# Kernel optimization log

Hardware: AMD Instinct MI355X
Metric: run time of the kernel (lower is better)

## Reference

```python
import jax, jax.numpy as jnp
import numpy as np

NUM_QUBITS = 4
NUM_LAYERS = 3
B = 16384


def ry(t):
    # t: scalar or [B] -> [2,2] or [B,2,2] complex64
    c = jnp.cos(t / 2)
    s = jnp.sin(t / 2)
    return jnp.stack([jnp.stack([c, -s], -1), jnp.stack([s, c], -1)], -2).astype(jnp.complex64)


def rz(t):
    e = jnp.exp(-0.5j * t.astype(jnp.complex64))
    z = jnp.zeros_like(e)
    return jnp.stack([jnp.stack([e, z], -1), jnp.stack([z, jnp.conj(e)], -1)], -2)


def apply_gate(psi, G, wire):
    # psi: [B,2,2,2,2]; G: [2,2] (shared) or [B,2,2] (per-sample)
    ax = 1 + wire
    psi = jnp.moveaxis(psi, ax, -1)
    if G.ndim == 3:
        psi = jnp.einsum('b...j,bij->b...i', psi, G)
    else:
        psi = jnp.einsum('...j,ij->...i', psi, G)
    return jnp.moveaxis(psi, -1, ax)


def cnot(psi, c, t):
    ca, ta = 1 + c, 1 + t
    p0 = jnp.take(psi, 0, axis=ca)
    p1 = jnp.take(psi, 1, axis=ca)
    p1 = jnp.flip(p1, axis=ta - (1 if ta > ca else 0))
    return jnp.stack([p0, p1], axis=ca)


def quantum_layer(inputs, qw):
    # inputs: [B,4] angles; qw: [3,4,2] circuit weights -> [B,4] PauliZ expvals
    b = inputs.shape[0]
    psi = jnp.zeros((b, 2, 2, 2, 2), jnp.complex64).at[:, 0, 0, 0, 0].set(1.0)
    for w in range(NUM_QUBITS):
        psi = apply_gate(psi, ry(inputs[:, w]), w)
    for l in range(NUM_LAYERS):
        for q in range(NUM_QUBITS):
            psi = apply_gate(psi, ry(qw[l, q, 0]), q)
            psi = apply_gate(psi, rz(qw[l, q, 1]), q)
        for q in range(NUM_QUBITS - 1):
            psi = cnot(psi, q, q + 1)
        psi = cnot(psi, NUM_QUBITS - 1, 0)
    pr = jnp.real(psi * jnp.conj(psi))  # [B,2,2,2,2]
    signs = jnp.array([1.0, -1.0], jnp.float32)
    outs = []
    for w in range(NUM_QUBITS):
        shp = [1, 1, 1, 1, 1]
        shp[1 + w] = 2
        outs.append(jnp.sum(pr * signs.reshape(shp), axis=(1, 2, 3, 4)))
    return jnp.stack(outs, axis=1).astype(jnp.float32)


def setup_inputs() -> dict:
    key = jax.random.key(0)
    ks = jax.random.split(key, 10)
    x = jax.random.normal(ks[0], (B, 1280), jnp.float32)
    W1 = jax.random.normal(ks[1], (1280, 64), jnp.float32) * 0.03
    b1 = jnp.zeros((64,), jnp.float32)
    W2 = jax.random.normal(ks[2], (64, 4), jnp.float32) * 0.12
    b2 = jnp.zeros((4,), jnp.float32)
    qw = jax.random.normal(ks[3], (NUM_LAYERS, NUM_QUBITS, 2), jnp.float32) * 0.1
    Wc1 = jax.random.normal(ks[4], (8, 16), jnp.float32) * 0.35
    bc1 = jnp.zeros((16,), jnp.float32)
    Wc2 = jax.random.normal(ks[5], (16, 1), jnp.float32) * 0.25
    bc2 = jnp.zeros((1,), jnp.float32)
    return {"x": x, "W1": W1, "b1": b1, "W2": W2, "b2": b2, "qw": qw,
            "Wc1": Wc1, "bc1": bc1, "Wc2": Wc2, "bc2": bc2}


def reference(x, W1, b1, W2, b2, qw, Wc1, bc1, Wc2, bc2):
    # reducer: 1280 -> 64 -> 4 with tanh (dropout inactive in eval)
    h = jax.nn.relu(x @ W1 + b1)
    reduced = jnp.tanh(h @ W2 + b2)  # [B,4]
    quantum_out = quantum_layer(reduced, qw)  # [B,4]
    combined = jnp.concatenate([reduced, quantum_out], axis=1)  # [B,8]
    logits = jax.nn.relu(combined @ Wc1 + bc1) @ Wc2 + bc2  # [B,1]
    return logits
```

## Files before the change

### kernel.cpp

```cpp
#include <hip/hip_runtime.h>
#include <math.h>

typedef __attribute__((ext_vector_type(4))) float f32x4;
typedef __attribute__((ext_vector_type(8))) short s16x8;

__device__ __forceinline__ short f2bf_rne(float f) {
  unsigned u = __float_as_uint(f);
  unsigned r = u + 0x7FFFu + ((u >> 16) & 1u);
  return (short)(r >> 16);
}
__device__ __forceinline__ float bf2f(short b) {
  return __uint_as_float(((unsigned)(unsigned short)b) << 16);
}

__global__ __launch_bounds__(256) void prep_w1(const float* __restrict__ W1,
                                               unsigned short* __restrict__ wf) {
  const int c   = blockIdx.x;
  const int l   = threadIdx.x & 63;
  const int nt  = threadIdx.x >> 6;
  const int kb  = c * 32 + (l >> 4) * 8;
  const int col = nt * 16 + (l & 15);
  s16x8 hi, lo;
#pragma unroll
  for (int j = 0; j < 8; ++j) {
    float f = W1[(kb + j) * 64 + col];
    short h = f2bf_rne(f);
    hi[j] = h;
    lo[j] = f2bf_rne(f - bf2f(h));
  }
  const int slot = (c * 4 + nt) * 2;
  *(s16x8*)(wf + (size_t)(slot * 64 + l) * 8)       = hi;
  *(s16x8*)(wf + (size_t)((slot + 1) * 64 + l) * 8) = lo;
}

#define APPLY_RY(BIT, C, S)                                                  \
  { _Pragma("unroll")                                                        \
    for (int i = 0; i < 16; ++i) {                                           \
      if (!(i & (BIT))) {                                                    \
        const int j = i | (BIT);                                             \
        float ar = re[i], ai = im[i], br = re[j], bi = im[j];                \
        re[i] = fmaf((C), ar, -(S) * br);                                    \
        im[i] = fmaf((C), ai, -(S) * bi);                                    \
        re[j] = fmaf((S), ar, (C) * br);                                     \
        im[j] = fmaf((S), ai, (C) * bi);                                     \
      }                                                                      \
    } }

#define APPLY_RZ(BIT, C, S)                                                  \
  { _Pragma("unroll")                                                        \
    for (int i = 0; i < 16; ++i) {                                           \
      float vr = re[i], vi = im[i];                                          \
      if (!(i & (BIT))) { re[i] = fmaf((C), vr, (S) * vi);                   \
                          im[i] = fmaf((C), vi, -(S) * vr); }                \
      else              { re[i] = fmaf((C), vr, -(S) * vi);                  \
                          im[i] = fmaf((C), vi, (S) * vr); }                 \
    } }

#define APPLY_CNOT(CB, TB)                                                   \
  { _Pragma("unroll")                                                        \
    for (int i = 0; i < 16; ++i) {                                           \
      if ((i & (CB)) && !(i & (TB))) {                                       \
        const int j = i | (TB);                                              \
        float t = re[i]; re[i] = re[j]; re[j] = t;                           \
        t = im[i]; im[i] = im[j]; im[j] = t;                                 \
      }                                                                      \
    } }

__global__ __launch_bounds__(256) void qfc_mfma4(
    const float* __restrict__ x,
    const unsigned short* __restrict__ wf,
    const float* __restrict__ b1, const float* __restrict__ W2,
    const float* __restrict__ b2, const float* __restrict__ qw,
    const float* __restrict__ Wc1, const float* __restrict__ bc1,
    const float* __restrict__ Wc2, const float* __restrict__ bc2,
    float* __restrict__ out) {
  __shared__ float lds[4096];

  const int tid  = threadIdx.x;
  const int l    = tid & 63;
  const int wv   = tid >> 6;
  const int r0   = blockIdx.x * 16;
  const int arow = l & 15;
  const int kg   = l >> 4;

  const float* xp = x + (size_t)(r0 + arow) * 1280 + wv * 320 + kg * 8;
  const s16x8* bw = (const s16x8*)wf + (size_t)wv * 5120 + l;

  f32x4 acc[4];
#pragma unroll
  for (int nt = 0; nt < 4; ++nt) acc[nt] = (f32x4)(0.f);

  float4 apf[4][2];
  s16x8  bpf[2][8];

#define LOAD_A(STG, C)                                        \
  { const float* p_ = xp + (C) * 32;                          \
    apf[STG][0] = *(const float4*)(p_);                       \
    apf[STG][1] = *(const float4*)(p_ + 4); }

#define LOAD_B(PAR, C)                                        \
  { const s16x8* bp_ = bw + (C) * 512;                        \
    _Pragma("unroll")                                         \
    for (int q_ = 0; q_ < 8; ++q_) bpf[PAR][q_] = bp_[q_ * 64]; }

  LOAD_A(0, 0) LOAD_A(1, 1) LOAD_A(2, 2) LOAD_A(3, 3)
  LOAD_B(0, 0) LOAD_B(1, 1)

#pragma unroll
  for (int c = 0; c < 10; ++c) {
    float f[8];
    f[0] = apf[c & 3][0].x; f[1] = apf[c & 3][0].y;
    f[2] = apf[c & 3][0].z; f[3] = apf[c & 3][0].w;
    f[4] = apf[c & 3][1].x; f[5] = apf[c & 3][1].y;
    f[6] = apf[c & 3][1].z; f[7] = apf[c & 3][1].w;
    s16x8 ah, al;
#pragma unroll
    for (int j = 0; j < 8; ++j) {
      short h = f2bf_rne(f[j]);
      ah[j] = h;
      al[j] = (short)(__float_as_uint(f[j] - bf2f(h)) >> 16);
    }
    if (c + 4 < 10) LOAD_A(c & 3, c + 4)

#pragma unroll
    for (int nt = 0; nt < 4; ++nt)
      acc[nt] = __builtin_amdgcn_mfma_f32_16x16x32_bf16(ah, bpf[c & 1][nt * 2], acc[nt], 0, 0, 0);
#pragma unroll
    for (int nt = 0; nt < 4; ++nt)
      acc[nt] = __builtin_amdgcn_mfma_f32_16x16x32_bf16(al, bpf[c & 1][nt * 2], acc[nt], 0, 0, 0);
#pragma unroll
    for (int nt = 0; nt < 4; ++nt)
      acc[nt] = __builtin_amdgcn_mfma_f32_16x16x32_bf16(ah, bpf[c & 1][nt * 2 + 1], acc[nt], 0, 0, 0);

    if (c + 2 < 10) LOAD_B(c & 1, c + 2)
  }
#undef LOAD_A
#undef LOAD_B

#pragma unroll
  for (int nt = 0; nt < 4; ++nt)
    *(float4*)&lds[wv * 1024 + (nt * 16 + arow) * 16 + kg * 4] =
        make_float4(acc[nt][0], acc[nt][1], acc[nt][2], acc[nt][3]);
  __syncthreads();

  if (tid < 64) {
    const int s  = tid >> 2;
    const int cq = tid & 3;

    float h4[4] = {0.f, 0.f, 0.f, 0.f};
#pragma unroll
    for (int cc = 0; cc < 16; ++cc) {
      const int c = cq * 16 + cc;
      const int o = c * 16 + s;
      float p  = (lds[o] + lds[1024 + o]) + (lds[2048 + o] + lds[3072 + o]);
      float hv = fmaxf(p + b1[c], 0.f);
      const float4 w2 = *(const float4*)(W2 + c * 4);
      h4[0] = fmaf(hv, w2.x, h4[0]);
      h4[1] = fmaf(hv, w2.y, h4[1]);
      h4[2] = fmaf(hv, w2.z, h4[2]);
      h4[3] = fmaf(hv, w2.w, h4[3]);
    }
#pragma unroll
    for (int k = 0; k < 4; ++k) {
      h4[k] += __shfl_xor(h4[k], 1);
      h4[k] += __shfl_xor(h4[k], 2);
    }

    float red[4];
#pragma unroll
    for (int k = 0; k < 4; ++k) red[k] = tanhf(h4[k] + b2[k]);

    float re[16], im[16];
#pragma unroll
    for (int i = 0; i < 16; ++i) { re[i] = 0.f; im[i] = 0.f; }
    re[0] = 1.f;
    {
      float s0, c0; sincosf(0.5f * red[0], &s0, &c0); APPLY_RY(8, c0, s0);
      float s1, c1; sincosf(0.5f * red[1], &s1, &c1); APPLY_RY(4, c1, s1);
      float s2, c2; sincosf(0.5f * red[2], &s2, &c2); APPLY_RY(2, c2, s2);
      float s3, c3; sincosf(0.5f * red[3], &s3, &c3); APPLY_RY(1, c3, s3);
    }
    for (int lyr = 0; lyr < 3; ++lyr) {
      const float* ql = qw + lyr * 8;
      { float sn, cn; sincosf(0.5f * ql[0], &sn, &cn); APPLY_RY(8, cn, sn); }
      { float sn, cn; sincosf(0.5f * ql[1], &sn, &cn); APPLY_RZ(8, cn, sn); }
      { float sn, cn; sincosf(0.5f * ql[2], &sn, &cn); APPLY_RY(4, cn, sn); }
      { float sn, cn; sincosf(0.5f * ql[3], &sn, &cn); APPLY_RZ(4, cn, sn); }
      { float sn, cn; sincosf(0.5f * ql[4], &sn, &cn); APPLY_RY(2, cn, sn); }
      { float sn, cn; sincosf(0.5f * ql[5], &sn, &cn); APPLY_RZ(2, cn, sn); }
      { float sn, cn; sincosf(0.5f * ql[6], &sn, &cn); APPLY_RY(1, cn, sn); }
      { float sn, cn; sincosf(0.5f * ql[7], &sn, &cn); APPLY_RZ(1, cn, sn); }
      APPLY_CNOT(8, 4);
      APPLY_CNOT(4, 2);
      APPLY_CNOT(2, 1);
      APPLY_CNOT(1, 8);
    }
    float q0 = 0.f, q1 = 0.f, q2 = 0.f, q3 = 0.f;
#pragma unroll
    for (int i = 0; i < 16; ++i) {
      const float pr = fmaf(re[i], re[i], im[i] * im[i]);
      q0 += (i & 8) ? -pr : pr;
      q1 += (i & 4) ? -pr : pr;
      q2 += (i & 2) ? -pr : pr;
      q3 += (i & 1) ? -pr : pr;
    }

    float logit = bc2[0];
#pragma unroll
    for (int j = 0; j < 16; ++j) {
      float a = bc1[j];
      a = fmaf(red[0], Wc1[j],       a);
      a = fmaf(red[1], Wc1[16 + j],  a);
      a = fmaf(red[2], Wc1[32 + j],  a);
      a = fmaf(red[3], Wc1[48 + j],  a);
      a = fmaf(q0,     Wc1[64 + j],  a);
      a = fmaf(q1,     Wc1[80 + j],  a);
      a = fmaf(q2,     Wc1[96 + j],  a);
      a = fmaf(q3,     Wc1[112 + j], a);
      logit = fmaf(fmaxf(a, 0.f), Wc2[j], logit);
    }
    if (cq == 0) out[r0 + s] = logit;
  }
}

#define NKT 20
__global__ __launch_bounds__(256) void qfc_fused(
    const float* __restrict__ x, const float* __restrict__ W1,
    const float* __restrict__ b1, const float* __restrict__ W2,
    const float* __restrict__ b2, const float* __restrict__ qw,
    const float* __restrict__ Wc1, const float* __restrict__ bc1,
    const float* __restrict__ Wc2, const float* __restrict__ bc2,
    float* __restrict__ out) {
  __shared__ float lds[16384];
  const int tid = threadIdx.x;
  const int lane = tid & 63;
  const int wv = tid >> 6;
  const int rg = lane >> 3;
  const int cg = lane & 7;
  const int r0 = blockIdx.x * 64;
  float acc[8][8];
#pragma unroll
  for (int i = 0; i < 8; ++i)
#pragma unroll
    for (int j = 0; j < 8; ++j) acc[i][j] = 0.f;
  const float* xrow = x + (size_t)(r0 + lane) * 1280 + wv * 16;
  const int aBase = wv * 1024;
  const int bBase = 8192 + wv * 1024;
  float4 a_st[4], b_st[4];
  auto issue_loads = [&](int kt) {
    const float* ap = xrow + kt * 64;
#pragma unroll
    for (int i = 0; i < 4; ++i) a_st[i] = *(const float4*)(ap + i * 4);
    const float* bp = W1 + kt * 4096 + wv * 1024 + lane * 4;
#pragma unroll
    for (int i = 0; i < 4; ++i) b_st[i] = *(const float4*)(bp + i * 256);
  };
  auto write_stage = [&](int buf) {
    float* A = &lds[buf * 4096 + aBase];
#pragma unroll
    for (int i = 0; i < 4; ++i) {
      float* p = A + i * 256 + lane;
      p[0] = a_st[i].x; p[64] = a_st[i].y; p[128] = a_st[i].z; p[192] = a_st[i].w;
    }
    float* Bp = &lds[buf * 4096 + bBase + lane * 4];
#pragma unroll
    for (int i = 0; i < 4; ++i) *(float4*)(Bp + i * 256) = b_st[i];
  };
  auto compute_tile = [&](int buf) {
#pragma unroll
    for (int m = 0; m < 16; ++m) {
      const float* Ak = &lds[buf * 4096 + aBase + m * 64];
      const float* Bk = &lds[buf * 4096 + bBase + m * 64];
      const float4 a0 = *(const float4*)(Ak + rg * 8);
      const float4 a1 = *(const float4*)(Ak + rg * 8 + 4);
      const float4 c0 = *(const float4*)(Bk + cg * 8);
      const float4 c1 = *(const float4*)(Bk + cg * 8 + 4);
      const float av[8] = {a0.x, a0.y, a0.z, a0.w, a1.x, a1.y, a1.z, a1.w};
      const float bv[8] = {c0.x, c0.y, c0.z, c0.w, c1.x, c1.y, c1.z, c1.w};
#pragma unroll
      for (int i = 0; i < 8; ++i)
#pragma unroll
        for (int j = 0; j < 8; ++j) acc[i][j] = fmaf(av[i], bv[j], acc[i][j]);
    }
  };
  issue_loads(0);
  write_stage(0);
  for (int kt = 0; kt < NKT; ++kt) {
    const int buf = kt & 1;
    if (kt + 1 < NKT) issue_loads(kt + 1);
    compute_tile(buf);
    if (kt + 1 < NKT) write_stage(buf ^ 1);
  }
  __syncthreads();
#pragma unroll
  for (int j = 0; j < 8; ++j) {
    const int c = cg * 8 + j;
    float* p = &lds[wv * 4096 + c * 64 + rg * 8];
    *(float4*)p = make_float4(acc[0][j], acc[1][j], acc[2][j], acc[3][j]);
    *(float4*)(p + 4) = make_float4(acc[4][j], acc[5][j], acc[6][j], acc[7][j]);
  }
  __syncthreads();
  const int s = tid >> 2;
  const int cq = tid & 3;
  float h4[4] = {0.f, 0.f, 0.f, 0.f};
#pragma unroll
  for (int cc = 0; cc < 16; ++cc) {
    const int c = cq * 16 + cc;
    const int o = c * 64 + s;
    float pp = (lds[o] + lds[4096 + o]) + (lds[8192 + o] + lds[12288 + o]);
    float hv = fmaxf(pp + b1[c], 0.f);
    const float4 w2 = *(const float4*)(W2 + c * 4);
    h4[0] = fmaf(hv, w2.x, h4[0]);
    h4[1] = fmaf(hv, w2.y, h4[1]);
    h4[2] = fmaf(hv, w2.z, h4[2]);
    h4[3] = fmaf(hv, w2.w, h4[3]);
  }
#pragma unroll
  for (int k = 0; k < 4; ++k) {
    h4[k] += __shfl_xor(h4[k], 1);
    h4[k] += __shfl_xor(h4[k], 2);
  }
  float red[4];
#pragma unroll
  for (int k = 0; k < 4; ++k) red[k] = tanhf(h4[k] + b2[k]);
  float re[16], im[16];
#pragma unroll
  for (int i = 0; i < 16; ++i) { re[i] = 0.f; im[i] = 0.f; }
  re[0] = 1.f;
  {
    float s0, c0; sincosf(0.5f * red[0], &s0, &c0); APPLY_RY(8, c0, s0);
    float s1, c1; sincosf(0.5f * red[1], &s1, &c1); APPLY_RY(4, c1, s1);
    float s2, c2; sincosf(0.5f * red[2], &s2, &c2); APPLY_RY(2, c2, s2);
    float s3, c3; sincosf(0.5f * red[3], &s3, &c3); APPLY_RY(1, c3, s3);
  }
  for (int lyr = 0; lyr < 3; ++lyr) {
    const float* ql = qw + lyr * 8;
    { float sn, cn; sincosf(0.5f * ql[0], &sn, &cn); APPLY_RY(8, cn, sn); }
    { float sn, cn; sincosf(0.5f * ql[1], &sn, &cn); APPLY_RZ(8, cn, sn); }
    { float sn, cn; sincosf(0.5f * ql[2], &sn, &cn); APPLY_RY(4, cn, sn); }
    { float sn, cn; sincosf(0.5f * ql[3], &sn, &cn); APPLY_RZ(4, cn, sn); }
    { float sn, cn; sincosf(0.5f * ql[4], &sn, &cn); APPLY_RY(2, cn, sn); }
    { float sn, cn; sincosf(0.5f * ql[5], &sn, &cn); APPLY_RZ(2, cn, sn); }
    { float sn, cn; sincosf(0.5f * ql[6], &sn, &cn); APPLY_RY(1, cn, sn); }
    { float sn, cn; sincosf(0.5f * ql[7], &sn, &cn); APPLY_RZ(1, cn, sn); }
    APPLY_CNOT(8, 4);
    APPLY_CNOT(4, 2);
    APPLY_CNOT(2, 1);
    APPLY_CNOT(1, 8);
  }
  float q0 = 0.f, q1 = 0.f, q2 = 0.f, q3 = 0.f;
#pragma unroll
  for (int i = 0; i < 16; ++i) {
    const float pr = fmaf(re[i], re[i], im[i] * im[i]);
    q0 += (i & 8) ? -pr : pr;
    q1 += (i & 4) ? -pr : pr;
    q2 += (i & 2) ? -pr : pr;
    q3 += (i & 1) ? -pr : pr;
  }
  float logit = bc2[0];
#pragma unroll
  for (int j = 0; j < 16; ++j) {
    float a = bc1[j];
    a = fmaf(red[0], Wc1[j],       a);
    a = fmaf(red[1], Wc1[16 + j],  a);
    a = fmaf(red[2], Wc1[32 + j],  a);
    a = fmaf(red[3], Wc1[48 + j],  a);
    a = fmaf(q0,     Wc1[64 + j],  a);
    a = fmaf(q1,     Wc1[80 + j],  a);
    a = fmaf(q2,     Wc1[96 + j],  a);
    a = fmaf(q3,     Wc1[112 + j], a);
    logit = fmaf(fmaxf(a, 0.f), Wc2[j], logit);
  }
  if (cq == 0) out[r0 + s] = logit;
}

extern "C" void kernel_launch(void* const* d_in, const int* in_sizes, int n_in,
                              void* d_out, int out_size, void* d_ws, size_t ws_size,
                              hipStream_t stream) {
  const float* x   = (const float*)d_in[0];
  const float* W1  = (const float*)d_in[1];
  const float* b1  = (const float*)d_in[2];
  const float* W2  = (const float*)d_in[3];
  const float* b2  = (const float*)d_in[4];
  const float* qw  = (const float*)d_in[5];
  const float* Wc1 = (const float*)d_in[6];
  const float* bc1 = (const float*)d_in[7];
  const float* Wc2 = (const float*)d_in[8];
  const float* bc2 = (const float*)d_in[9];

  if (ws_size >= 327680) {
    unsigned short* wf = (unsigned short*)d_ws;
    prep_w1<<<dim3(40), dim3(256), 0, stream>>>(W1, wf);
    qfc_mfma4<<<dim3(1024), dim3(256), 0, stream>>>(
        x, wf, b1, W2, b2, qw, Wc1, bc1, Wc2, bc2, (float*)d_out);
  } else {
    qfc_fused<<<dim3(256), dim3(256), 0, stream>>>(
        x, W1, b1, W2, b2, qw, Wc1, bc1, Wc2, bc2, (float*)d_out);
  }
}
```

Baseline: 40.52 us.

## Split GEMM into LDS-staged kernel with partial-sum buffer and separate tail kernel

The fused GEMM+quantum kernel is split in two. The GEMM kernel gives each block a 64-row tile and one quarter of K, double-buffers x and W1 fragments into LDS with global_load_lds, and writes partial sums to a 16 MB workspace. A second kernel reduces the four K-partials and runs the whole tail on all 256 threads, where the old kernel used only 64. This aims to raise memory-load efficiency and tail parallelism, at the cost of an extra launch and a large partial-sum write and read.

```diff
diff --git a/kernel.cpp b/kernel.cpp
--- a/kernel.cpp
+++ b/kernel.cpp
@@ -11,6 +11,16 @@
 }
 __device__ __forceinline__ float bf2f(short b) {
   return __uint_as_float(((unsigned)(unsigned short)b) << 16);
+}
+
+#define WAIT_VMCNT(N) asm volatile("s_waitcnt vmcnt(" #N ")" ::: "memory")
+#define WAIT_LGKM0()  asm volatile("s_waitcnt lgkmcnt(0)" ::: "memory")
+#define BAR()         __builtin_amdgcn_s_barrier()
+
+__device__ __forceinline__ void gl_lds16(const void* g, void* l) {
+  __builtin_amdgcn_global_load_lds(
+      (const __attribute__((address_space(1))) void*)g,
+      (__attribute__((address_space(3))) void*)l, 16, 0, 0);
 }
 
 __global__ __launch_bounds__(256) void prep_w1(const float* __restrict__ W1,
@@ -66,16 +76,185 @@
       }                                                                      \
     } }
 
-__global__ __launch_bounds__(256) void qfc_mfma4(
+__global__ __launch_bounds__(256) void qfc_gemm(
     const float* __restrict__ x,
     const unsigned short* __restrict__ wf,
+    float* __restrict__ pw)
+{
+  __shared__ s16x8 Bs[2][512];
+  __shared__ float As[2][4][512];
+
+  const int tid  = threadIdx.x;
+  const int l    = tid & 63;
+  const int wv   = tid >> 6;
+  const int rt   = blockIdx.x >> 2;
+  const int kq   = blockIdx.x & 3;
+  const int arow = l & 15;
+  const int kg   = l >> 4;
+
+  const float* xw = x + (size_t)(rt * 64 + wv * 16 + (l >> 2)) * 1280 +
+                    kq * 320 + (l & 3) * 4;
+  const s16x8* wfch = (const s16x8*)wf + (size_t)(kq * 10) * 512;
+
+  f32x4 acc[4];
+#pragma unroll
+  for (int nt = 0; nt < 4; ++nt) acc[nt] = (f32x4)(0.f);
+
+#define STAGE(C, BUF)                                                        \
+  {                                                                          \
+    const s16x8* bsrc_ = wfch + (size_t)(C) * 512 + wv * 128 + l;            \
+    gl_lds16(bsrc_,      &Bs[BUF][wv * 128]);                                \
+    gl_lds16(bsrc_ + 64, &Bs[BUF][wv * 128 + 64]);                           \
+    const float* asrc_ = xw + (C) * 32;                                      \
+    gl_lds16(asrc_,      &As[BUF][wv][0]);                                   \
+    gl_lds16(asrc_ + 16, &As[BUF][wv][256]);                                 \
+  }
+
+  STAGE(0, 0)
+  STAGE(1, 1)
+
+#pragma unroll
+  for (int c = 0; c < 10; ++c) {
+    const int buf = c & 1;
+    if (c < 9) { WAIT_VMCNT(4); } else { WAIT_VMCNT(0); }
+    BAR();
+
+    const float* Ab = &As[buf][wv][(kg >> 1) * 256 + arow * 16 + (kg & 1) * 8];
+    const float4 fa = *(const float4*)(Ab);
+    const float4 fb = *(const float4*)(Ab + 4);
+    float f[8] = {fa.x, fa.y, fa.z, fa.w, fb.x, fb.y, fb.z, fb.w};
+    s16x8 ah, al;
+#pragma unroll
+    for (int j = 0; j < 8; ++j) {
+      short h = f2bf_rne(f[j]);
+      ah[j] = h;
+      al[j] = (short)(__float_as_uint(f[j] - bf2f(h)) >> 16);
+    }
+    s16x8 bq[8];
+#pragma unroll
+    for (int q = 0; q < 8; ++q) bq[q] = Bs[buf][q * 64 + l];
+
+    WAIT_LGKM0();
+    if (c + 2 < 10) {
+      BAR();
+      STAGE(c + 2, buf)
+    }
+
+#pragma unroll
+    for (int nt = 0; nt < 4; ++nt)
+      acc[nt] = __builtin_amdgcn_mfma_f32_16x16x32_bf16(ah, bq[nt * 2], acc[nt], 0, 0, 0);
+#pragma unroll
+    for (int nt = 0; nt < 4; ++nt)
+      acc[nt] = __builtin_amdgcn_mfma_f32_16x16x32_bf16(al, bq[nt * 2], acc[nt], 0, 0, 0);
+#pragma unroll
+    for (int nt = 0; nt < 4; ++nt)
+      acc[nt] = __builtin_amdgcn_mfma_f32_16x16x32_bf16(ah, bq[nt * 2 + 1], acc[nt], 0, 0, 0);
+  }
+#undef STAGE
+
+  float* wsp = pw + (size_t)blockIdx.x * 4096;
+#pragma unroll
+  for (int nt = 0; nt < 4; ++nt)
+    *(float4*)(wsp + (nt * 16 + arow) * 64 + wv * 16 + kg * 4) =
+        make_float4(acc[nt][0], acc[nt][1], acc[nt][2], acc[nt][3]);
+}
+
+__global__ __launch_bounds__(256) void qfc_tail(
+    const float* __restrict__ pw,
+    const float* __restrict__ b1, const float* __restrict__ W2,
+    const float* __restrict__ b2, const float* __restrict__ qw,
+    const float* __restrict__ Wc1, const float* __restrict__ bc1,
+    const float* __restrict__ Wc2, const float* __restrict__ bc2,
+    float* __restrict__ out) {
+  const int tid = threadIdx.x;
+  const int s   = tid >> 2;
+  const int cq  = tid & 3;
+  const int rt  = blockIdx.x;
+  const float* base = pw + (size_t)rt * 4 * 4096;
+
+  float h4[4] = {0.f, 0.f, 0.f, 0.f};
+#pragma unroll
+  for (int cc = 0; cc < 16; ++cc) {
+    const int c = cq * 16 + cc;
+    const int o = c * 64 + s;
+    float p  = (base[o] + base[4096 + o]) + (base[8192 + o] + base[12288 + o]);
+    float hv = fmaxf(p + b1[c], 0.f);
+    const float4 w2 = *(const float4*)(W2 + c * 4);
+    h4[0] = fmaf(hv, w2.x, h4[0]);
+    h4[1] = fmaf(hv, w2.y, h4[1]);
+    h4[2] = fmaf(hv, w2.z, h4[2]);
+    h4[3] = fmaf(hv, w2.w, h4[3]);
+  }
+#pragma unroll
+  for (int k = 0; k < 4; ++k) {
+    h4[k] += __shfl_xor(h4[k], 1);
+    h4[k] += __shfl_xor(h4[k], 2);
+  }
+
+  float red[4];
+#pragma unroll
+  for (int k = 0; k < 4; ++k) red[k] = tanhf(h4[k] + b2[k]);
+
+  float re[16], im[16];
+#pragma unroll
+  for (int i = 0; i < 16; ++i) { re[i] = 0.f; im[i] = 0.f; }
+  re[0] = 1.f;
+  {
+    float s0, c0; sincosf(0.5f * red[0], &s0, &c0); APPLY_RY(8, c0, s0);
+    float s1, c1; sincosf(0.5f * red[1], &s1, &c1); APPLY_RY(4, c1, s1);
+    float s2, c2; sincosf(0.5f * red[2], &s2, &c2); APPLY_RY(2, c2, s2);
+    float s3, c3; sincosf(0.5f * red[3], &s3, &c3); APPLY_RY(1, c3, s3);
+  }
+  for (int lyr = 0; lyr < 3; ++lyr) {
+    const float* ql = qw + lyr * 8;
+    { float sn, cn; sincosf(0.5f * ql[0], &sn, &cn); APPLY_RY(8, cn, sn); }
+    { float sn, cn; sincosf(0.5f * ql[1], &sn, &cn); APPLY_RZ(8, cn, sn); }
+    { float sn, cn; sincosf(0.5f * ql[2], &sn, &cn); APPLY_RY(4, cn, sn); }
+    { float sn, cn; sincosf(0.5f * ql[3], &sn, &cn); APPLY_RZ(4, cn, sn); }
+    { float sn, cn; sincosf(0.5f * ql[4], &sn, &cn); APPLY_RY(2, cn, sn); }
+    { float sn, cn; sincosf(0.5f * ql[5], &sn, &cn); APPLY_RZ(2, cn, sn); }
+    { float sn, cn; sincosf(0.5f * ql[6], &sn, &cn); APPLY_RY(1, cn, sn); }
+    { float sn, cn; sincosf(0.5f * ql[7], &sn, &cn); APPLY_RZ(1, cn, sn); }
+    APPLY_CNOT(8, 4);
+    APPLY_CNOT(4, 2);
+    APPLY_CNOT(2, 1);
+    APPLY_CNOT(1, 8);
+  }
+  float q0 = 0.f, q1 = 0.f, q2 = 0.f, q3 = 0.f;
+#pragma unroll
+  for (int i = 0; i < 16; ++i) {
+    const float pr = fmaf(re[i], re[i], im[i] * im[i]);
+    q0 += (i & 8) ? -pr : pr;
+    q1 += (i & 4) ? -pr : pr;
+    q2 += (i & 2) ? -pr : pr;
+    q3 += (i & 1) ? -pr : pr;
+  }
+
+  float logit = bc2[0];
+#pragma unroll
+  for (int j = 0; j < 16; ++j) {
+    float a = bc1[j];
+    a = fmaf(red[0], Wc1[j],       a);
+    a = fmaf(red[1], Wc1[16 + j],  a);
+    a = fmaf(red[2], Wc1[32 + j],  a);
+    a = fmaf(red[3], Wc1[48 + j],  a);
+    a = fmaf(q0,     Wc1[64 + j],  a);
+    a = fmaf(q1,     Wc1[80 + j],  a);
+    a = fmaf(q2,     Wc1[96 + j],  a);
+    a = fmaf(q3,     Wc1[112 + j], a);
+    logit = fmaf(fmaxf(a, 0.f), Wc2[j], logit);
+  }
+  if (cq == 0) out[rt * 64 + s] = logit;
+}
+
+__global__ __launch_bounds__(256) void qfc_mfma4(
+    const float* __restrict__ x, const unsigned short* __restrict__ wf,
     const float* __restrict__ b1, const float* __restrict__ W2,
     const float* __restrict__ b2, const float* __restrict__ qw,
     const float* __restrict__ Wc1, const float* __restrict__ bc1,
     const float* __restrict__ Wc2, const float* __restrict__ bc2,
     float* __restrict__ out) {
   __shared__ float lds[4096];
-
   const int tid  = threadIdx.x;
   const int l    = tid & 63;
   const int wv   = tid >> 6;
@@ -89,23 +268,18 @@
   f32x4 acc[4];
 #pragma unroll
   for (int nt = 0; nt < 4; ++nt) acc[nt] = (f32x4)(0.f);
-
   float4 apf[4][2];
   s16x8  bpf[2][8];
-
 #define LOAD_A(STG, C)                                        \
   { const float* p_ = xp + (C) * 32;                          \
     apf[STG][0] = *(const float4*)(p_);                       \
     apf[STG][1] = *(const float4*)(p_ + 4); }
-
 #define LOAD_B(PAR, C)                                        \
   { const s16x8* bp_ = bw + (C) * 512;                        \
     _Pragma("unroll")                                         \
     for (int q_ = 0; q_ < 8; ++q_) bpf[PAR][q_] = bp_[q_ * 64]; }
-
   LOAD_A(0, 0) LOAD_A(1, 1) LOAD_A(2, 2) LOAD_A(3, 3)
   LOAD_B(0, 0) LOAD_B(1, 1)
-
 #pragma unroll
   for (int c = 0; c < 10; ++c) {
     float f[8];
@@ -121,7 +295,6 @@
       al[j] = (short)(__float_as_uint(f[j] - bf2f(h)) >> 16);
     }
     if (c + 4 < 10) LOAD_A(c & 3, c + 4)
-
 #pragma unroll
     for (int nt = 0; nt < 4; ++nt)
       acc[nt] = __builtin_amdgcn_mfma_f32_16x16x32_bf16(ah, bpf[c & 1][nt * 2], acc[nt], 0, 0, 0);
@@ -131,22 +304,18 @@
 #pragma unroll
     for (int nt = 0; nt < 4; ++nt)
       acc[nt] = __builtin_amdgcn_mfma_f32_16x16x32_bf16(ah, bpf[c & 1][nt * 2 + 1], acc[nt], 0, 0, 0);
-
     if (c + 2 < 10) LOAD_B(c & 1, c + 2)
   }
 #undef LOAD_A
 #undef LOAD_B
-
 #pragma unroll
   for (int nt = 0; nt < 4; ++nt)
     *(float4*)&lds[wv * 1024 + (nt * 16 + arow) * 16 + kg * 4] =
         make_float4(acc[nt][0], acc[nt][1], acc[nt][2], acc[nt][3]);
   __syncthreads();
-
   if (tid < 64) {
     const int s  = tid >> 2;
     const int cq = tid & 3;
-
     float h4[4] = {0.f, 0.f, 0.f, 0.f};
 #pragma unroll
     for (int cc = 0; cc < 16; ++cc) {
@@ -165,11 +334,9 @@
       h4[k] += __shfl_xor(h4[k], 1);
       h4[k] += __shfl_xor(h4[k], 2);
     }
-
     float red[4];
 #pragma unroll
     for (int k = 0; k < 4; ++k) red[k] = tanhf(h4[k] + b2[k]);
-
     float re[16], im[16];
 #pragma unroll
     for (int i = 0; i < 16; ++i) { re[i] = 0.f; im[i] = 0.f; }
@@ -204,7 +371,6 @@
       q2 += (i & 2) ? -pr : pr;
       q3 += (i & 1) ? -pr : pr;
     }
-
     float logit = bc2[0];
 #pragma unroll
     for (int j = 0; j < 16; ++j) {
@@ -388,7 +554,16 @@
   const float* Wc2 = (const float*)d_in[8];
   const float* bc2 = (const float*)d_in[9];
 
-  if (ws_size >= 327680) {
+  const size_t WF_BYTES = 327680;
+  const size_t PW_BYTES = (size_t)1024 * 4096 * 4;
+  if (ws_size >= WF_BYTES + PW_BYTES) {
+    unsigned short* wf = (unsigned short*)d_ws;
+    float* pw = (float*)((char*)d_ws + WF_BYTES);
+    prep_w1<<<dim3(40), dim3(256), 0, stream>>>(W1, wf);
+    qfc_gemm<<<dim3(1024), dim3(256), 0, stream>>>(x, wf, pw);
+    qfc_tail<<<dim3(256), dim3(256), 0, stream>>>(
+        pw, b1, W2, b2, qw, Wc1, bc1, Wc2, bc2, (float*)d_out);
+  } else if (ws_size >= WF_BYTES) {
     unsigned short* wf = (unsigned short*)d_ws;
     prep_w1<<<dim3(40), dim3(256), 0, stream>>>(W1, wf);
     qfc_mfma4<<<dim3(1024), dim3(256), 0, stream>>>(
```

Result: no change. 39.92 us (-1.5%).
